# Kernel optimization log

Hardware: AMD Instinct MI355X
Metric: run time of the kernel (lower is better)

## Reference

```python
import jax, jax.numpy as jnp
import numpy as np

B, C = 4194304, 8
ALPHA, GAMMA = 0.25, 2.0  # dynamic values at training_step=0
TASK_WEIGHTS = {"direction": 1.0, "volatility": 0.5}


def setup_inputs() -> dict:
    key = jax.random.key(0)
    k1, k2, k3, k4 = jax.random.split(key, 4)
    return {
        "logits_direction": jax.random.normal(k1, (B, C), dtype=jnp.float32),
        "labels_direction": jax.random.randint(k2, (B,), 0, C, dtype=jnp.int32),
        "logits_volatility": jax.random.normal(k3, (B, C), dtype=jnp.float32),
        "labels_volatility": jax.random.randint(k4, (B,), 0, C, dtype=jnp.int32),
    }


def _focal_task_loss(logits, labels):
    # softmax over classes, gather p_t for the true class
    probs = jax.nn.softmax(logits, axis=1)                      # [B, C]
    pt = jnp.take_along_axis(probs, labels[:, None], axis=1)[:, 0]  # [B]
    alpha_t = jnp.where(labels == 0, 1.0 - ALPHA, ALPHA)
    focal_w = jnp.power(1.0 - pt, GAMMA)
    loss = -alpha_t * focal_w * jnp.log(pt + 1e-8)
    loss = jnp.where(labels == 1, loss * 1.5, loss)             # boost class-1 samples
    return jnp.mean(loss)


def reference(logits_direction, labels_direction, logits_volatility, labels_volatility):
    l_dir = _focal_task_loss(logits_direction, labels_direction)
    l_vol = _focal_task_loss(logits_volatility, labels_volatility)
    total = TASK_WEIGHTS["direction"] * l_dir + TASK_WEIGHTS["volatility"] * l_vol
    # [total_loss, loss_direction, loss_volatility]
    return jnp.stack([total, l_dir, l_vol])
```

## Files before the change

### kernel.cpp

```cpp
#include <hip/hip_runtime.h>


#define B_ROWS 4194304
#define NB 1024

__global__ __launch_bounds__(256) void focal_partial_kernel(
    const float* __restrict__ logits_dir, const int* __restrict__ labels_dir,
    const float* __restrict__ logits_vol, const int* __restrict__ labels_vol,
    float* __restrict__ partials )
{
    const int task = blockIdx.y;
    const float* __restrict__ logits = task ? logits_vol : logits_dir;
    const int*   __restrict__ labels = task ? labels_vol : labels_dir;

    float acc = 0.0f;
    const int stride = NB * 256;
    for (int r = blockIdx.x * 256 + threadIdx.x; r < B_ROWS; r += stride) {
        const float4 a = *reinterpret_cast<const float4*>(logits + (size_t)r * 8);
        const float4 b = *reinterpret_cast<const float4*>(logits + (size_t)r * 8 + 4);
        const int lab = labels[r];

        const float x0 = a.x, x1 = a.y, x2 = a.z, x3 = a.w;
        const float x4 = b.x, x5 = b.y, x6 = b.z, x7 = b.w;

        const float m = fmaxf(fmaxf(fmaxf(x0, x1), fmaxf(x2, x3)),
                              fmaxf(fmaxf(x4, x5), fmaxf(x6, x7)));
        const float e0 = expf(x0 - m), e1 = expf(x1 - m);
        const float e2 = expf(x2 - m), e3 = expf(x3 - m);
        const float e4 = expf(x4 - m), e5 = expf(x5 - m);
        const float e6 = expf(x6 - m), e7 = expf(x7 - m);
        const float s = ((e0 + e1) + (e2 + e3)) + ((e4 + e5) + (e6 + e7));

        float xl = x0;
        xl = (lab == 1) ? x1 : xl;
        xl = (lab == 2) ? x2 : xl;
        xl = (lab == 3) ? x3 : xl;
        xl = (lab == 4) ? x4 : xl;
        xl = (lab == 5) ? x5 : xl;
        xl = (lab == 6) ? x6 : xl;
        xl = (lab == 7) ? x7 : xl;

        const float pt = expf(xl - m) * (1.0f / s);
        const float alpha_t = (lab == 0) ? 0.75f : 0.25f;
        const float omp = 1.0f - pt;
        const float focal_w = omp * omp;
        float loss = -alpha_t * focal_w * logf(pt + 1e-8f);
        loss = (lab == 1) ? loss * 1.5f : loss;
        acc += loss;
    }

    #pragma unroll
    for (int off = 32; off > 0; off >>= 1)
        acc += __shfl_down(acc, off);

    __shared__ float lds[4];
    const int lane = threadIdx.x & 63;
    const int wid  = threadIdx.x >> 6;
    if (lane == 0) lds[wid] = acc;
    __syncthreads();
    if (threadIdx.x == 0) {
        const float bsum = (lds[0] + lds[1]) + (lds[2] + lds[3]);
        partials[task * NB + blockIdx.x] = bsum;
    }
}

__global__ __launch_bounds__(256) void focal_final_kernel(
    const float* __restrict__ partials, float* __restrict__ out)
{
    double sd = 0.0, sv = 0.0;
    for (int k = threadIdx.x; k < NB; k += 256) {
        sd += (double)partials[k];
        sv += (double)partials[NB + k];
    }
    #pragma unroll
    for (int off = 32; off > 0; off >>= 1) {
        sd += __shfl_down(sd, off);
        sv += __shfl_down(sv, off);
    }
    __shared__ double lds[8];
    const int lane = threadIdx.x & 63;
    const int wid  = threadIdx.x >> 6;
    if (lane == 0) { lds[wid] = sd; lds[4 + wid] = sv; }
    __syncthreads();
    if (threadIdx.x == 0) {
        const double l_dir = ((lds[0] + lds[1]) + (lds[2] + lds[3])) / (double)B_ROWS;
        const double l_vol = ((lds[4] + lds[5]) + (lds[6] + lds[7])) / (double)B_ROWS;
        out[0] = (float)(l_dir + 0.5 * l_vol);
        out[1] = (float)l_dir;
        out[2] = (float)l_vol;
    }
}

extern "C" void kernel_launch(void* const* d_in, const int* in_sizes, int n_in,
                              void* d_out, int out_size, void* d_ws, size_t ws_size,
                              hipStream_t stream) {
    const float* logits_dir = (const float*)d_in[0];
    const int*   labels_dir = (const int*)d_in[1];
    const float* logits_vol = (const float*)d_in[2];
    const int*   labels_vol = (const int*)d_in[3];
    float* out = (float*)d_out;
    float* partials = (float*)d_ws;

    dim3 grid(NB, 2);
    focal_partial_kernel<<<grid, 256, 0, stream>>>(logits_dir, labels_dir,
                                                   logits_vol, labels_vol, partials);
    focal_final_kernel<<<1, 256, 0, stream>>>(partials, out);
}
```

Before: 302.8 us.

## Split rows across lane pairs with DPP and software-pipeline inline-asm loads

Each lane now processes half a row as one contiguous 16-byte load. Row max, sum and true-class exp are combined across the lane pair with DPP xor swizzles, so every wave reads a fully contiguous 1 KB chunk. Loads are issued through inline global_load asm with a four-deep rotating buffer and explicit vmcnt waits, keeping several chunks in flight while earlier ones are computed. Math switches to hardware exp2, log and rcp intrinsics. Because both lanes of a pair add the same loss, the final mean divides by twice the row count.

```diff
diff --git a/kernel.cpp b/kernel.cpp
--- a/kernel.cpp
+++ b/kernel.cpp
@@ -1,10 +1,58 @@
 #include <hip/hip_runtime.h>
 
 
+typedef float v4f __attribute__((ext_vector_type(4)));
+
 #define B_ROWS 4194304
 #define NB 1024
+#define LOG2E 1.4426950408889634f
+#define LN2   0.6931471805599453f
 
-__global__ __launch_bounds__(256) void focal_partial_kernel(
+__device__ __forceinline__ float xor1f(float x) {
+    int yi = __builtin_amdgcn_update_dpp(0, __builtin_bit_cast(int, x),
+                                         0xB1 , 0xF, 0xF, true);
+    return __builtin_bit_cast(float, yi);
+}
+
+__device__ __forceinline__ void issue_chunk(v4f& q, int& lab,
+                                            unsigned voff_log, unsigned voff_lab,
+                                            const float* lbase, const int* labase) {
+    asm volatile("global_load_dwordx4 %0, %1, %2"
+                 : "=&v"(q) : "v"(voff_log), "s"(lbase));
+    asm volatile("global_load_dword %0, %1, %2"
+                 : "=&v"(lab) : "v"(voff_lab), "s"(labase));
+}
+
+#define WAIT_VM(N) do { asm volatile("s_waitcnt vmcnt(" #N ")"); \
+                        __builtin_amdgcn_sched_barrier(0); } while (0)
+
+__device__ __forceinline__ float half_row_loss(const v4f q, const int lab,
+                                               const int cls_base) {
+    const float m4 = fmaxf(fmaxf(q.x, q.y), fmaxf(q.z, q.w));
+    const float m  = fmaxf(m4, xor1f(m4));
+    const float mL = m * LOG2E;
+    const float e0 = __builtin_amdgcn_exp2f(__builtin_fmaf(q.x, LOG2E, -mL));
+    const float e1 = __builtin_amdgcn_exp2f(__builtin_fmaf(q.y, LOG2E, -mL));
+    const float e2 = __builtin_amdgcn_exp2f(__builtin_fmaf(q.z, LOG2E, -mL));
+    const float e3 = __builtin_amdgcn_exp2f(__builtin_fmaf(q.w, LOG2E, -mL));
+    const float s4 = (e0 + e1) + (e2 + e3);
+    const float s  = s4 + xor1f(s4);
+    float el4 = 0.0f;
+    el4 = (lab == cls_base + 0) ? e0 : el4;
+    el4 = (lab == cls_base + 1) ? e1 : el4;
+    el4 = (lab == cls_base + 2) ? e2 : el4;
+    el4 = (lab == cls_base + 3) ? e3 : el4;
+    const float el = el4 + xor1f(el4);
+    const float pt = el * __builtin_amdgcn_rcpf(s);
+    float c = (lab == 0) ? (0.75f * LN2) : (0.25f * LN2);
+    c = (lab == 1) ? (0.375f * LN2) : c;
+    const float omp = 1.0f - pt;
+    const float w = omp * omp;
+    const float lg = __builtin_amdgcn_logf(pt + 1e-8f);
+    return -(c * w) * lg;
+}
+
+__global__ __launch_bounds__(256, 8) void focal_partial_kernel(
     const float* __restrict__ logits_dir, const int* __restrict__ labels_dir,
     const float* __restrict__ logits_vol, const int* __restrict__ labels_vol,
     float* __restrict__ partials )
@@ -13,41 +61,31 @@
     const float* __restrict__ logits = task ? logits_vol : logits_dir;
     const int*   __restrict__ labels = task ? labels_vol : labels_dir;
 
+    const int tid = threadIdx.x;
+    const int gid = blockIdx.x * 256 + tid;
+    const int W = gid >> 6;
+    const int l = tid & 63;
+    const int cls_base = (l & 1) * 4;
+    const unsigned voff_log0 = (unsigned)W * 32768u + (unsigned)l * 16u;
+    const unsigned voff_lab0 = (unsigned)W * 4096u  + (unsigned)(l >> 1) * 4u;
+
+    v4f Q[4]; int L[4];
+    issue_chunk(Q[0], L[0], voff_log0,          voff_lab0,        logits, labels);
+    issue_chunk(Q[1], L[1], voff_log0 + 1024u,  voff_lab0 + 128u, logits, labels);
+    issue_chunk(Q[2], L[2], voff_log0 + 2048u,  voff_lab0 + 256u, logits, labels);
+
     float acc = 0.0f;
-    const int stride = NB * 256;
-    for (int r = blockIdx.x * 256 + threadIdx.x; r < B_ROWS; r += stride) {
-        const float4 a = *reinterpret_cast<const float4*>(logits + (size_t)r * 8);
-        const float4 b = *reinterpret_cast<const float4*>(logits + (size_t)r * 8 + 4);
-        const int lab = labels[r];
-
-        const float x0 = a.x, x1 = a.y, x2 = a.z, x3 = a.w;
-        const float x4 = b.x, x5 = b.y, x6 = b.z, x7 = b.w;
-
-        const float m = fmaxf(fmaxf(fmaxf(x0, x1), fmaxf(x2, x3)),
-                              fmaxf(fmaxf(x4, x5), fmaxf(x6, x7)));
-        const float e0 = expf(x0 - m), e1 = expf(x1 - m);
-        const float e2 = expf(x2 - m), e3 = expf(x3 - m);
-        const float e4 = expf(x4 - m), e5 = expf(x5 - m);
-        const float e6 = expf(x6 - m), e7 = expf(x7 - m);
-        const float s = ((e0 + e1) + (e2 + e3)) + ((e4 + e5) + (e6 + e7));
-
-        float xl = x0;
-        xl = (lab == 1) ? x1 : xl;
-        xl = (lab == 2) ? x2 : xl;
-        xl = (lab == 3) ? x3 : xl;
-        xl = (lab == 4) ? x4 : xl;
-        xl = (lab == 5) ? x5 : xl;
-        xl = (lab == 6) ? x6 : xl;
-        xl = (lab == 7) ? x7 : xl;
-
-        const float pt = expf(xl - m) * (1.0f / s);
-        const float alpha_t = (lab == 0) ? 0.75f : 0.25f;
-        const float omp = 1.0f - pt;
-        const float focal_w = omp * omp;
-        float loss = -alpha_t * focal_w * logf(pt + 1e-8f);
-        loss = (lab == 1) ? loss * 1.5f : loss;
-        acc += loss;
+    #pragma unroll
+    for (int j = 0; j <= 28; ++j) {
+        issue_chunk(Q[(j + 3) & 3], L[(j + 3) & 3],
+                    voff_log0 + (unsigned)(j + 3) * 1024u,
+                    voff_lab0 + (unsigned)(j + 3) * 128u, logits, labels);
+        WAIT_VM(6);
+        acc += half_row_loss(Q[j & 3], L[j & 3], cls_base);
     }
+    WAIT_VM(4); acc += half_row_loss(Q[29 & 3], L[29 & 3], cls_base);
+    WAIT_VM(2); acc += half_row_loss(Q[30 & 3], L[30 & 3], cls_base);
+    WAIT_VM(0); acc += half_row_loss(Q[31 & 3], L[31 & 3], cls_base);
 
     #pragma unroll
     for (int off = 32; off > 0; off >>= 1)
@@ -83,8 +121,8 @@
     if (lane == 0) { lds[wid] = sd; lds[4 + wid] = sv; }
     __syncthreads();
     if (threadIdx.x == 0) {
-        const double l_dir = ((lds[0] + lds[1]) + (lds[2] + lds[3])) / (double)B_ROWS;
-        const double l_vol = ((lds[4] + lds[5]) + (lds[6] + lds[7])) / (double)B_ROWS;
+        const double l_dir = ((lds[0] + lds[1]) + (lds[2] + lds[3])) / (2.0 * (double)B_ROWS);
+        const double l_vol = ((lds[4] + lds[5]) + (lds[6] + lds[7])) / (2.0 * (double)B_ROWS);
         out[0] = (float)(l_dir + 0.5 * l_vol);
         out[1] = (float)l_dir;
         out[2] = (float)l_vol;
```

Result: faster. 295.7 us (-2.3%).
